# Kernel optimization log

Hardware: AMD Instinct MI355X
Metric: run time of the kernel (lower is better)

## Reference

```python
import jax, jax.numpy as jnp
import numpy as np

BATCH, SEQ, N_INPUT, N_HIDDEN, N_OUTPUT = 256, 512, 512, 128, 2


def setup_inputs() -> dict:
    key = jax.random.key(0)
    ks = jax.random.split(key, 6)
    s_i = 1.0 / np.sqrt(N_INPUT)
    s_h = 1.0 / np.sqrt(N_HIDDEN)
    return {
        "x": jax.random.normal(ks[0], (BATCH, SEQ, N_INPUT), dtype=jnp.float32),
        # LSTM gate kernels, gate order (i, f, g, o) concatenated on last axis.
        # flax nn.LSTMCell: dense_i has no bias, dense_h has bias.
        "Wi": jax.random.normal(ks[1], (N_INPUT, 4 * N_HIDDEN), dtype=jnp.float32) * s_i,
        "Wh": jax.random.normal(ks[2], (N_HIDDEN, 4 * N_HIDDEN), dtype=jnp.float32) * s_h,
        "b": jax.random.normal(ks[3], (4 * N_HIDDEN,), dtype=jnp.float32) * 0.01,
        "Wd": jax.random.normal(ks[4], (N_HIDDEN, N_OUTPUT), dtype=jnp.float32) * s_h,
        "bd": jax.random.normal(ks[5], (N_OUTPUT,), dtype=jnp.float32) * 0.01,
    }


def reference(x, Wi, Wh, b, Wd, bd):
    B, S, _ = x.shape
    H = Wh.shape[0]
    # Precompute input projection for all steps in one big GEMM: (S, B, 4H)
    x_gates = jnp.einsum('bsi,ig->sbg', x, Wi)

    def step(carry, xg):
        c, h = carry
        gates = xg + h @ Wh + b  # (B, 4H)
        i, f, g, o = jnp.split(gates, 4, axis=-1)
        c = jax.nn.sigmoid(f) * c + jax.nn.sigmoid(i) * jnp.tanh(g)
        h = jax.nn.sigmoid(o) * jnp.tanh(c)
        return (c, h), h

    c0 = jnp.zeros((B, H), dtype=x.dtype)
    h0 = jnp.zeros((B, H), dtype=x.dtype)
    (_, h_last), _ = jax.lax.scan(step, (c0, h0), x_gates)
    logits = h_last @ Wd + bd  # (B, N_OUTPUT)
    return logits
```

## Files before the change

kernel.cpp:

```cpp
#include <hip/hip_runtime.h>
#include <hip/hip_bf16.h>


typedef __attribute__((ext_vector_type(8))) short short8;
typedef __attribute__((ext_vector_type(4))) float floatx4;
typedef __attribute__((ext_vector_type(4))) unsigned short ushortx4;
typedef __attribute__((ext_vector_type(4))) unsigned int uintx4;

#define LOG2E 1.44269504088896340736f

__device__ __forceinline__ unsigned short f2bf(float f) {
  unsigned int u = __builtin_bit_cast(unsigned int, f);
  u = (u + 0x7fffu + ((u >> 16) & 1u)) >> 16;
  return (unsigned short)u;
}
__device__ __forceinline__ float bf2f(unsigned short u) {
  unsigned int v = ((unsigned int)u) << 16;
  return __builtin_bit_cast(float, v);
}
__device__ __forceinline__ float sigf(float x) {
  return __builtin_amdgcn_rcpf(1.0f + __builtin_amdgcn_exp2f(-LOG2E * x));
}
__device__ __forceinline__ float tanhf_(float x) {
  return 1.0f - 2.0f * __builtin_amdgcn_rcpf(1.0f + __builtin_amdgcn_exp2f(2.0f * LOG2E * x));
}
__device__ __forceinline__ void bar_lds() {
  asm volatile("s_waitcnt lgkmcnt(0)" ::: "memory");
  __builtin_amdgcn_s_barrier();
}
__device__ __forceinline__ void gl_lds16(const void* g, void* l) {
  __builtin_amdgcn_global_load_lds(
      (const __attribute__((address_space(1))) unsigned int*)g,
      (__attribute__((address_space(3))) unsigned int*)l, 16, 0, 0);
}

__global__ void pack_kernel(const float* __restrict__ Wi, const float* __restrict__ Wh,
                            unsigned short* __restrict__ Wi_p, unsigned short* __restrict__ Wh_p) {
  int idx = blockIdx.x * 256 + threadIdx.x;
  if (idx < 262144) {
    int j = idx & 7, lane = (idx >> 3) & 63, nt = (idx >> 9) & 31, kk = idx >> 14;
    int k = kk * 32 + ((lane >> 4) * 8) + j;
    int n = nt * 16 + (lane & 15);
    Wi_p[idx] = f2bf(Wi[k * 512 + n]);
  } else {
    int i2 = idx - 262144;
    int j = i2 & 7, lane = (i2 >> 3) & 63, nt = (i2 >> 9) & 31, kk = i2 >> 14;
    int k = kk * 32 + ((lane >> 4) * 8) + j;
    int n = nt * 16 + (lane & 15);
    Wh_p[i2] = f2bf(Wh[k * 512 + n]);
  }
}

__global__ __launch_bounds__(512, 2) void xgemm_kernel(
    const float* __restrict__ x, const unsigned short* __restrict__ Wi_p,
    const float* __restrict__ bias, unsigned int* __restrict__ xg4) {
  __shared__ __align__(16) unsigned short As[128 * 72];
  __shared__ __align__(16) unsigned short Bs[2 * 32 * 64 * 8];

  const int tid = threadIdx.x;
  const int lane = tid & 63;
  const int w = tid >> 6;
  const int wm = w >> 2, wn = w & 3;
  const int quad = lane >> 4;
  const int lm = lane & 15;
  const int bm = blockIdx.x;
  const int s = bm >> 1;
  const int b0 = (bm & 1) * 128;

  float bs_[4][2];
  #pragma unroll
  for (int g = 0; g < 4; ++g)
    #pragma unroll
    for (int jc = 0; jc < 2; ++jc)
      bs_[g][jc] = bias[g * 128 + wn * 32 + jc * 16 + lm];

  floatx4 acc[4][8];
  #pragma unroll
  for (int a = 0; a < 4; ++a)
    #pragma unroll
    for (int b2 = 0; b2 < 8; ++b2) { acc[a][b2].x = 0.f; acc[a][b2].y = 0.f; acc[a][b2].z = 0.f; acc[a][b2].w = 0.f; }

  const float* xbase = x + ((size_t)(b0 + w * 16 + quad) * 512 + s) * 512 + lm * 4;

  for (int kt = 0; kt < 8; ++kt) {
    __syncthreads();
    #pragma unroll
    for (int c = 0; c < 8; ++c) {
      int kg = c & 1, ntl = (c >> 1) * 8 + w;
      const unsigned short* src = Wi_p + ((size_t)((kt * 2 + kg) * 32 + ntl) * 64 + lane) * 8;
      unsigned short* dst = &Bs[(size_t)((kg * 32 + ntl) * 64) * 8];
      gl_lds16(src, dst);
    }
    #pragma unroll
    for (int i = 0; i < 4; ++i) {
      floatx4 v = *(const floatx4*)(xbase + (size_t)i * 1048576 + kt * 64);
      int r = w * 16 + i * 4 + quad;
      ushortx4 u;
      u.x = f2bf(v.x); u.y = f2bf(v.y); u.z = f2bf(v.z); u.w = f2bf(v.w);
      *(ushortx4*)(&As[r * 72 + lm * 4]) = u;
    }
    __syncthreads();
    #pragma unroll
    for (int ks = 0; ks < 2; ++ks) {
      short8 af[4];
      #pragma unroll
      for (int mt = 0; mt < 4; ++mt) {
        int m = wm * 64 + mt * 16 + lm;
        af[mt] = *(const short8*)(&As[m * 72 + ks * 32 + quad * 8]);
      }
      #pragma unroll
      for (int nt = 0; nt < 8; ++nt) {
        int g = nt >> 1, jc = nt & 1;
        int ntl = g * 8 + wn * 2 + jc;
        short8 bfv = *(const short8*)(&Bs[(size_t)((ks * 32 + ntl) * 64 + lane) * 8]);
        #pragma unroll
        for (int mt = 0; mt < 4; ++mt)
          acc[mt][nt] = __builtin_amdgcn_mfma_f32_16x16x32_bf16(af[mt], bfv, acc[mt][nt], 0, 0, 0);
      }
    }
  }
  #pragma unroll
  for (int mt = 0; mt < 4; ++mt) {
    int bbv = ((b0 + wm * 64 + mt * 16) >> 2) + quad;
    #pragma unroll
    for (int jc = 0; jc < 2; ++jc) {
      int jj = wn * 32 + jc * 16 + lm;
      #pragma unroll
      for (int rh = 0; rh < 2; ++rh) {
        uintx4 v;
        #pragma unroll
        for (int g = 0; g < 4; ++g) {
          float lo = acc[mt][g * 2 + jc][rh]     + bs_[g][jc];
          float hi2 = acc[mt][g * 2 + jc][rh + 2] + bs_[g][jc];
          v[g] = (unsigned int)f2bf(lo) | ((unsigned int)f2bf(hi2) << 16);
        }
        *(uintx4*)(xg4 + ((((size_t)s * 64 + bbv) * 2 + rh) * 128 + jj) * 4) = v;
      }
    }
  }
}

__global__ __launch_bounds__(512, 2) void lstm_kernel(
    const unsigned int* __restrict__ xg4, const unsigned short* __restrict__ Wh_p,
    const float* __restrict__ Wd, const float* __restrict__ bd,
    float* __restrict__ out) {
  __shared__ __align__(16) unsigned short hb[2 * 16 * 138];
  __shared__ __align__(16) float gb[128 * 20];

  const int tid = threadIdx.x;
  const int lane = tid & 63;
  const int w = tid >> 6;
  const int quad = lane >> 4;
  const int lm = lane & 15;
  const int bb = blockIdx.x;

  for (int i = tid; i < 2 * 16 * 138; i += 512) hb[i] = 0;

  short8 bfr[4][4];
  #pragma unroll
  for (int kk = 0; kk < 4; ++kk)
    #pragma unroll
    for (int tt = 0; tt < 4; ++tt)
      bfr[kk][tt] = *(const short8*)(Wh_p + ((size_t)(kk * 32 + tt * 8 + w) * 64 + lane) * 8);

  const int r0 = w >> 2;
  const int jj = (w & 3) * 32 + (lane & 31);
  const int hi = lane >> 5;
  const int row = r0 + 2 * hi;
  float cst = 0.f;

  const unsigned int* xp = xg4 + ((size_t)(bb * 2 + r0) * 128 + jj) * 4;
  uintx4 xga = *(const uintx4*)(xp);
  uintx4 xgb = *(const uintx4*)(xp + 65536);

  const unsigned int* hbu = (const unsigned int*)hb;

  __syncthreads();

  auto substep = [&](const int rp, uintx4& xcur, int spre) {
    uintx4 xv = xcur;
    if (spre < 512)
      xcur = *(const uintx4*)(xp + (size_t)spre * 65536);

    short8 af[4];
    #pragma unroll
    for (int kk = 0; kk < 4; ++kk) {
      union { short8 v; unsigned int u[4]; } t;
      #pragma unroll
      for (int i = 0; i < 4; ++i)
        t.u[i] = hbu[rp * 1104 + lm * 69 + kk * 16 + quad * 4 + i];
      af[kk] = t.v;
    }
    floatx4 acc[4];
    #pragma unroll
    for (int tt = 0; tt < 4; ++tt) { acc[tt].x = 0.f; acc[tt].y = 0.f; acc[tt].z = 0.f; acc[tt].w = 0.f; }
    #pragma unroll
    for (int kk = 0; kk < 4; ++kk)
      #pragma unroll
      for (int tt = 0; tt < 4; ++tt)
        acc[tt] = __builtin_amdgcn_mfma_f32_16x16x32_bf16(af[kk], bfr[kk][tt], acc[tt], 0, 0, 0);
    if (lane < 16) {
      #pragma unroll
      for (int r = 0; r < 4; ++r) {
        floatx4 gv;
        gv.x = acc[0][r]; gv.y = acc[1][r]; gv.z = acc[2][r]; gv.w = acc[3][r];
        *(floatx4*)(gb + (w * 16 + lm) * 20 + r * 4) = gv;
      }
    }
    bar_lds();

    floatx4 gv = *(const floatx4*)(gb + jj * 20 + row * 4);
    float pre[4];
    #pragma unroll
    for (int g = 0; g < 4; ++g) {
      unsigned int u = xv[g];
      unsigned short xvs = hi ? (unsigned short)(u >> 16) : (unsigned short)(u & 0xffffu);
      pre[g] = gv[g] + bf2f(xvs);
    }
    float cc = sigf(pre[1]) * cst + sigf(pre[0]) * tanhf_(pre[2]);
    cst = cc;
    float hv = sigf(pre[3]) * tanhf_(cc);
    hb[(rp ^ 1) * 2208 + row * 138 + jj] = f2bf(hv);
    bar_lds();
  };

  for (int s = 0; s < 512; s += 2) {
    substep(0, xga, s + 2);
    substep(1, xgb, s + 3);
  }

  if (tid < 8) {
    int rw = tid >> 1, co = tid & 1;
    float a = bd[co];
    for (int j2 = 0; j2 < 128; ++j2)
      a += bf2f(hb[rw * 138 + j2]) * Wd[j2 * 2 + co];
    out[(bb * 4 + rw) * 2 + co] = a;
  }
}

extern "C" void kernel_launch(void* const* d_in, const int* in_sizes, int n_in,
                              void* d_out, int out_size, void* d_ws, size_t ws_size,
                              hipStream_t stream) {
  const float* x  = (const float*)d_in[0];
  const float* Wi = (const float*)d_in[1];
  const float* Wh = (const float*)d_in[2];
  const float* b  = (const float*)d_in[3];
  const float* Wd = (const float*)d_in[4];
  const float* bd = (const float*)d_in[5];
  float* out = (float*)d_out;

  unsigned short* Wi_p = (unsigned short*)d_ws;
  unsigned short* Wh_p = Wi_p + 262144;
  unsigned int*   xg4  = (unsigned int*)(Wh_p + 65536);

  pack_kernel<<<1280, 256, 0, stream>>>(Wi, Wh, Wi_p, Wh_p);
  xgemm_kernel<<<1024, 512, 0, stream>>>(x, Wi_p, b, xg4);
  lstm_kernel<<<64, 512, 0, stream>>>(xg4, Wh_p, Wd, bd, out);
}
```

Measured before the change: 804.5 us.

## Remove per-step block barrier in LSTM via wave-local gate exchange, prefetch x in GEMM

The LSTM recurrence kernel is reorganised so each wave owns a 16-column hidden slice for all four gates. The gate transpose through shared memory now stays within a wave, which removes one of the two block-wide barriers per timestep. The xg intermediate layout is changed so each thread reads one 8-byte packed gate vector, and the h buffer pitch becomes 140 so vector LDS reads work. The input GEMM also register-prefetches the next x tile before the MFMA loop to overlap global loads with compute. The risk is correctness if the within-wave LDS exchange relies on waitcnt alone without a barrier.

```diff
diff --git a/kernel.cpp b/kernel.cpp
--- a/kernel.cpp
+++ b/kernel.cpp
@@ -5,7 +5,7 @@
 typedef __attribute__((ext_vector_type(8))) short short8;
 typedef __attribute__((ext_vector_type(4))) float floatx4;
 typedef __attribute__((ext_vector_type(4))) unsigned short ushortx4;
-typedef __attribute__((ext_vector_type(4))) unsigned int uintx4;
+typedef __attribute__((ext_vector_type(2))) unsigned int uint2v;
 
 #define LOG2E 1.44269504088896340736f
 
@@ -53,7 +53,7 @@
 
 __global__ __launch_bounds__(512, 2) void xgemm_kernel(
     const float* __restrict__ x, const unsigned short* __restrict__ Wi_p,
-    const float* __restrict__ bias, unsigned int* __restrict__ xg4) {
+    const float* __restrict__ bias, unsigned int* __restrict__ xg5) {
   __shared__ __align__(16) unsigned short As[128 * 72];
   __shared__ __align__(16) unsigned short Bs[2 * 32 * 64 * 8];
 
@@ -82,8 +82,20 @@
 
   const float* xbase = x + ((size_t)(b0 + w * 16 + quad) * 512 + s) * 512 + lm * 4;
 
+  floatx4 cur[4], nxt[4];
+  #pragma unroll
+  for (int i = 0; i < 4; ++i)
+    cur[i] = *(const floatx4*)(xbase + (size_t)i * 1048576);
+
   for (int kt = 0; kt < 8; ++kt) {
-    __syncthreads();
+    bar_lds();
+    #pragma unroll
+    for (int i = 0; i < 4; ++i) {
+      int r = w * 16 + i * 4 + quad;
+      ushortx4 u;
+      u.x = f2bf(cur[i].x); u.y = f2bf(cur[i].y); u.z = f2bf(cur[i].z); u.w = f2bf(cur[i].w);
+      *(ushortx4*)(&As[r * 72 + lm * 4]) = u;
+    }
     #pragma unroll
     for (int c = 0; c < 8; ++c) {
       int kg = c & 1, ntl = (c >> 1) * 8 + w;
@@ -91,15 +103,15 @@
       unsigned short* dst = &Bs[(size_t)((kg * 32 + ntl) * 64) * 8];
       gl_lds16(src, dst);
     }
-    #pragma unroll
-    for (int i = 0; i < 4; ++i) {
-      floatx4 v = *(const floatx4*)(xbase + (size_t)i * 1048576 + kt * 64);
-      int r = w * 16 + i * 4 + quad;
-      ushortx4 u;
-      u.x = f2bf(v.x); u.y = f2bf(v.y); u.z = f2bf(v.z); u.w = f2bf(v.w);
-      *(ushortx4*)(&As[r * 72 + lm * 4]) = u;
-    }
-    __syncthreads();
+    if (kt < 7) {
+      #pragma unroll
+      for (int i = 0; i < 4; ++i)
+        nxt[i] = *(const floatx4*)(xbase + (size_t)i * 1048576 + (kt + 1) * 64);
+      asm volatile("s_waitcnt vmcnt(4) lgkmcnt(0)" ::: "memory");
+    } else {
+      asm volatile("s_waitcnt vmcnt(0) lgkmcnt(0)" ::: "memory");
+    }
+    __builtin_amdgcn_s_barrier();
     #pragma unroll
     for (int ks = 0; ks < 2; ++ks) {
       short8 af[4];
@@ -118,34 +130,37 @@
           acc[mt][nt] = __builtin_amdgcn_mfma_f32_16x16x32_bf16(af[mt], bfv, acc[mt][nt], 0, 0, 0);
       }
     }
+    #pragma unroll
+    for (int i = 0; i < 4; ++i) cur[i] = nxt[i];
   }
   #pragma unroll
   for (int mt = 0; mt < 4; ++mt) {
-    int bbv = ((b0 + wm * 64 + mt * 16) >> 2) + quad;
+    int bbase = b0 + wm * 64 + mt * 16 + quad * 4;
     #pragma unroll
     for (int jc = 0; jc < 2; ++jc) {
-      int jj = wn * 32 + jc * 16 + lm;
-      #pragma unroll
-      for (int rh = 0; rh < 2; ++rh) {
-        uintx4 v;
-        #pragma unroll
-        for (int g = 0; g < 4; ++g) {
-          float lo = acc[mt][g * 2 + jc][rh]     + bs_[g][jc];
-          float hi2 = acc[mt][g * 2 + jc][rh + 2] + bs_[g][jc];
-          v[g] = (unsigned int)f2bf(lo) | ((unsigned int)f2bf(hi2) << 16);
-        }
-        *(uintx4*)(xg4 + ((((size_t)s * 64 + bbv) * 2 + rh) * 128 + jj) * 4) = v;
+      int wv = wn * 2 + jc;
+      #pragma unroll
+      for (int rr = 0; rr < 4; ++rr) {
+        size_t cell = ((size_t)s * 64 + ((bbase + rr) >> 2)) * 512 + wv * 64 + rr * 16 + lm;
+        float g0 = acc[mt][0 + jc][rr] + bs_[0][jc];
+        float g1 = acc[mt][2 + jc][rr] + bs_[1][jc];
+        float g2 = acc[mt][4 + jc][rr] + bs_[2][jc];
+        float g3 = acc[mt][6 + jc][rr] + bs_[3][jc];
+        uint2v v;
+        v.x = (unsigned int)f2bf(g0) | ((unsigned int)f2bf(g1) << 16);
+        v.y = (unsigned int)f2bf(g2) | ((unsigned int)f2bf(g3) << 16);
+        *(uint2v*)(xg5 + cell * 2) = v;
       }
     }
   }
 }
 
 __global__ __launch_bounds__(512, 2) void lstm_kernel(
-    const unsigned int* __restrict__ xg4, const unsigned short* __restrict__ Wh_p,
+    const unsigned int* __restrict__ xg5, const unsigned short* __restrict__ Wh_p,
     const float* __restrict__ Wd, const float* __restrict__ bd,
     float* __restrict__ out) {
-  __shared__ __align__(16) unsigned short hb[2 * 16 * 138];
-  __shared__ __align__(16) float gb[128 * 20];
+  __shared__ __align__(16) unsigned short hb[2 * 16 * 140];
+  __shared__ __align__(16) float gbw[8 * 320];
 
   const int tid = threadIdx.x;
   const int lane = tid & 63;
@@ -154,73 +169,67 @@
   const int lm = lane & 15;
   const int bb = blockIdx.x;
 
-  for (int i = tid; i < 2 * 16 * 138; i += 512) hb[i] = 0;
+  for (int i = tid; i < 2 * 16 * 140; i += 512) hb[i] = 0;
 
   short8 bfr[4][4];
   #pragma unroll
   for (int kk = 0; kk < 4; ++kk)
     #pragma unroll
-    for (int tt = 0; tt < 4; ++tt)
-      bfr[kk][tt] = *(const short8*)(Wh_p + ((size_t)(kk * 32 + tt * 8 + w) * 64 + lane) * 8);
-
-  const int r0 = w >> 2;
-  const int jj = (w & 3) * 32 + (lane & 31);
-  const int hi = lane >> 5;
-  const int row = r0 + 2 * hi;
+    for (int g = 0; g < 4; ++g)
+      bfr[kk][g] = *(const short8*)(Wh_p + ((size_t)(kk * 32 + g * 8 + w) * 64 + lane) * 8);
+
   float cst = 0.f;
 
-  const unsigned int* xp = xg4 + ((size_t)(bb * 2 + r0) * 128 + jj) * 4;
-  uintx4 xga = *(const uintx4*)(xp);
-  uintx4 xgb = *(const uintx4*)(xp + 65536);
-
-  const unsigned int* hbu = (const unsigned int*)hb;
+  const unsigned int* xp = xg5 + ((size_t)bb * 512 + tid) * 2;
+  uint2v xga = *(const uint2v*)(xp);
+  uint2v xgb = *(const uint2v*)(xp + 65536);
+
+  float* gw = gbw + w * 320;
 
   __syncthreads();
 
-  auto substep = [&](const int rp, uintx4& xcur, int spre) {
-    uintx4 xv = xcur;
+  auto substep = [&](const int rp, uint2v& xcur, int spre) {
+    uint2v xv = xcur;
     if (spre < 512)
-      xcur = *(const uintx4*)(xp + (size_t)spre * 65536);
+      xcur = *(const uint2v*)(xp + (size_t)spre * 65536);
 
     short8 af[4];
     #pragma unroll
     for (int kk = 0; kk < 4; ++kk) {
-      union { short8 v; unsigned int u[4]; } t;
-      #pragma unroll
-      for (int i = 0; i < 4; ++i)
-        t.u[i] = hbu[rp * 1104 + lm * 69 + kk * 16 + quad * 4 + i];
+      const unsigned short* p = &hb[rp * 2240 + lm * 140 + kk * 32 + quad * 8];
+      union { short8 v; ushortx4 h[2]; } t;
+      t.h[0] = *(const ushortx4*)(p);
+      t.h[1] = *(const ushortx4*)(p + 4);
       af[kk] = t.v;
     }
     floatx4 acc[4];
     #pragma unroll
-    for (int tt = 0; tt < 4; ++tt) { acc[tt].x = 0.f; acc[tt].y = 0.f; acc[tt].z = 0.f; acc[tt].w = 0.f; }
+    for (int g = 0; g < 4; ++g) { acc[g].x = 0.f; acc[g].y = 0.f; acc[g].z = 0.f; acc[g].w = 0.f; }
     #pragma unroll
     for (int kk = 0; kk < 4; ++kk)
       #pragma unroll
-      for (int tt = 0; tt < 4; ++tt)
-        acc[tt] = __builtin_amdgcn_mfma_f32_16x16x32_bf16(af[kk], bfr[kk][tt], acc[tt], 0, 0, 0);
+      for (int g = 0; g < 4; ++g)
+        acc[g] = __builtin_amdgcn_mfma_f32_16x16x32_bf16(af[kk], bfr[kk][g], acc[g], 0, 0, 0);
+
     if (lane < 16) {
       #pragma unroll
       for (int r = 0; r < 4; ++r) {
-        floatx4 gv;
-        gv.x = acc[0][r]; gv.y = acc[1][r]; gv.z = acc[2][r]; gv.w = acc[3][r];
-        *(floatx4*)(gb + (w * 16 + lm) * 20 + r * 4) = gv;
-      }
-    }
-    bar_lds();
-
-    floatx4 gv = *(const floatx4*)(gb + jj * 20 + row * 4);
-    float pre[4];
-    #pragma unroll
-    for (int g = 0; g < 4; ++g) {
-      unsigned int u = xv[g];
-      unsigned short xvs = hi ? (unsigned short)(u >> 16) : (unsigned short)(u & 0xffffu);
-      pre[g] = gv[g] + bf2f(xvs);
-    }
-    float cc = sigf(pre[1]) * cst + sigf(pre[0]) * tanhf_(pre[2]);
+        floatx4 t4;
+        t4.x = acc[0][r]; t4.y = acc[1][r]; t4.z = acc[2][r]; t4.w = acc[3][r];
+        *(floatx4*)(gw + lm * 20 + r * 4) = t4;
+      }
+    }
+    asm volatile("s_waitcnt lgkmcnt(0)" ::: "memory");
+    floatx4 gv = *(const floatx4*)(gw + lm * 20 + quad * 4);
+
+    float pre0 = gv.x + bf2f((unsigned short)(xv.x & 0xffffu));
+    float pre1 = gv.y + bf2f((unsigned short)(xv.x >> 16));
+    float pre2 = gv.z + bf2f((unsigned short)(xv.y & 0xffffu));
+    float pre3 = gv.w + bf2f((unsigned short)(xv.y >> 16));
+    float cc = sigf(pre1) * cst + sigf(pre0) * tanhf_(pre2);
     cst = cc;
-    float hv = sigf(pre[3]) * tanhf_(cc);
-    hb[(rp ^ 1) * 2208 + row * 138 + jj] = f2bf(hv);
+    float hv = sigf(pre3) * tanhf_(cc);
+    hb[(rp ^ 1) * 2240 + quad * 140 + w * 16 + lm] = f2bf(hv);
     bar_lds();
   };
 
@@ -233,7 +242,7 @@
     int rw = tid >> 1, co = tid & 1;
     float a = bd[co];
     for (int j2 = 0; j2 < 128; ++j2)
-      a += bf2f(hb[rw * 138 + j2]) * Wd[j2 * 2 + co];
+      a += bf2f(hb[rw * 140 + j2]) * Wd[j2 * 2 + co];
     out[(bb * 4 + rw) * 2 + co] = a;
   }
 }
@@ -251,9 +260,9 @@
 
   unsigned short* Wi_p = (unsigned short*)d_ws;
   unsigned short* Wh_p = Wi_p + 262144;
-  unsigned int*   xg4  = (unsigned int*)(Wh_p + 65536);
+  unsigned int*   xg5  = (unsigned int*)(Wh_p + 65536);
 
   pack_kernel<<<1280, 256, 0, stream>>>(Wi, Wh, Wi_p, Wh_p);
-  xgemm_kernel<<<1024, 512, 0, stream>>>(x, Wi_p, b, xg4);
-  lstm_kernel<<<64, 512, 0, stream>>>(xg4, Wh_p, Wd, bd, out);
-}
+  xgemm_kernel<<<1024, 512, 0, stream>>>(x, Wi_p, b, xg5);
+  lstm_kernel<<<64, 512, 0, stream>>>(xg5, Wh_p, Wd, bd, out);
+}
```

After: 752.6 us. 6.4% less time.
